# Kernel optimization log

Measured on AMD Instinct MI355X. Metric: run time of the kernel, lower is better.

Reference implementation:

```python
import jax, jax.numpy as jnp
import numpy as np

N, D_IN, D_OUT = 4096, 1024, 1024
DROPOUT_RATE = 0.1


def setup_inputs() -> dict:
    key = jax.random.key(0)
    kx, kq, kk, kv = jax.random.split(key, 4)
    s = 1.0 / np.sqrt(D_IN)
    return {
        "x": jax.random.normal(kx, (N, D_IN), dtype=jnp.float32),
        "wq": jax.random.normal(kq, (D_OUT, D_IN), dtype=jnp.float32) * s,
        "wk": jax.random.normal(kk, (D_OUT, D_IN), dtype=jnp.float32) * s,
        "wv": jax.random.normal(kv, (D_OUT, D_IN), dtype=jnp.float32) * s,
    }


def reference(x, wq, wk, wv):
    # torch Linear: y = x @ W.T  (no bias since qkv_bias=False)
    q = x @ wq.T                      # [N, d_out]
    k = x @ wk.T
    v = x @ wv.T
    scores = q @ k.T                  # [N, N]
    n = scores.shape[0]
    causal = jnp.tril(jnp.ones((n, n), dtype=bool))  # keep lower triangle
    masked = jnp.where(causal, scores, -jnp.inf)
    scale = k.shape[-1] ** 0.5
    weights = jax.nn.softmax(masked / scale, axis=-1)
    # dropout (train mode), fixed key for determinism
    keep = jax.random.bernoulli(jax.random.key(42), 1.0 - DROPOUT_RATE, weights.shape)
    weights = jnp.where(keep, weights / (1.0 - DROPOUT_RATE), 0.0)
    return weights @ v                # [N, d_out]
```

## Files before the change

### kernel.cpp

```cpp
#include <hip/hip_runtime.h>
#include <hip/hip_fp16.h>

typedef __attribute__((ext_vector_type(8))) _Float16 f16x8;
typedef __attribute__((ext_vector_type(4))) float f32x4;

typedef const __attribute__((address_space(1))) void gas_void;
typedef __attribute__((address_space(3))) void las_void;
typedef __attribute__((address_space(3))) const __half las_chalf;

__device__ __forceinline__ f16x8 ldsr(const __half* p) {
    f16x8 r;
    asm volatile("ds_read_b128 %0, %1" : "=v"(r) : "v"((las_chalf*)p));
    return r;
}

__global__ __launch_bounds__(256) void cast_all_k(const float* __restrict__ x,
                                                  const float* __restrict__ wq,
                                                  const float* __restrict__ wk,
                                                  const float* __restrict__ wv,
                                                  __half* __restrict__ xb,
                                                  __half* __restrict__ wqkv) {
    const int b = blockIdx.x;
    const float* src;
    __half* dst;
    size_t i;
    if (b < 2048) {
        src = x; dst = xb;
        i = ((size_t)b * 256 + threadIdx.x) * 8;
    } else {
        const int w = (b - 2048) >> 9;
        src = w == 0 ? wq : (w == 1 ? wk : wv);
        dst = wqkv + (size_t)w * 1048576;
        i = (((size_t)((b - 2048) & 511)) * 256 + threadIdx.x) * 8;
    }
    float4 a = *(const float4*)(src + i);
    float4 c = *(const float4*)(src + i + 4);
    __half2 h[4] = { __floats2half2_rn(a.x, a.y), __floats2half2_rn(a.z, a.w),
                     __floats2half2_rn(c.x, c.y), __floats2half2_rn(c.z, c.w) };
    *(int4*)(dst + i) = *(int4*)h;
}

template <int MODE>
__global__ __launch_bounds__(512, 2)
void gemm256(const __half* __restrict__ pA, const __half* __restrict__ pB,
             void* __restrict__ pC, void* __restrict__ pC2,
             float* __restrict__ P1, float* __restrict__ P2, float* __restrict__ P3,
             const float* __restrict__ Lr) {
    constexpr int LDA = (MODE == 0) ? 1024 : (MODE == 1 ? 2048 : 4096);
    constexpr int LDB = (MODE == 0) ? 1024 : (MODE == 1 ? 2048 : 4096);
    constexpr float SCALE = (MODE == 1) ? 0.03125f : 1.0f;

    int bi, bj, c = 0, k_lo = 0, NT = 16;
    bool isVT = false;
    if constexpr (MODE == 0) {
        const int id = blockIdx.x;
        const int sw = (id & 7) * 24 + (id >> 3);
        if (sw < 128) { bi = sw >> 3; bj = sw & 7; }
        else          { int s2 = sw - 128; bi = s2 >> 4; bj = s2 & 15; isVT = true; }
    } else if constexpr (MODE == 1) {
        const int id = blockIdx.x;
        const int sw = (id & 7) * 17 + (id >> 3);
        int b = (int)((sqrtf(8.0f * sw + 1.0f) - 1.0f) * 0.5f);
        while ((b + 1) * (b + 2) / 2 <= sw) ++b;
        while (b * (b + 1) / 2 > sw) --b;
        bi = b; bj = sw - b * (b + 1) / 2;
    } else {
        const int id = blockIdx.x;
        const int sw = (id & 7) * 20 + (id >> 3);
        bj = sw / 40;
        const int x = sw - 40 * bj;
        if (x < 4)       { bi = x;                    c = 0; }
        else if (x < 12) { bi = 4  + ((x - 4) >> 1);  c = (x - 4) & 1; }
        else if (x < 24) { bi = 8  + (x - 12) / 3;    c = (x - 12) % 3; }
        else             { bi = 12 + ((x - 24) >> 2); c = (x - 24) & 3; }
        const int full = 4 * (bi + 1);
        k_lo = c * 16;
        NT = min(full - k_lo, 16);
    }

    const __half* A = pA;
    const __half* B = pB;
    if constexpr (MODE == 0) {
        if (isVT) { A = pB + 2097152; B = pA; }
    }

    const int brow = bi * 256, bcol = bj * 256;
    const int tid = threadIdx.x;
    const int lane = tid & 63, wid = tid >> 6;
    const int wm = wid >> 2, wn = wid & 3;
    const int lane15 = lane & 15;
    const int kxor = (lane & 7) << 3;
    const int g16 = (lane >> 4) << 3;

    extern __shared__ __half smem[];

    const int srow = (wid << 3) + (lane >> 3);
    const int scol = ((lane & 7) ^ ((lane >> 3) & 7)) << 3;

    auto stage_half = [&](const __half* G, int ldg, int growbase, int kt, int buf, int mat, int half) {
        const __half* src = G + (size_t)(growbase + half * 128 + srow) * ldg + kt * 64 + scol;
        __half* dst = &smem[buf * 32768 + mat * 16384 + (half * 128 + (wid << 3)) * 64];
        __builtin_amdgcn_global_load_lds((gas_void*)src, (las_void*)dst, 16, 0, 0);
        __builtin_amdgcn_global_load_lds((gas_void*)(src + (size_t)64 * ldg),
                                         (las_void*)(dst + 64 * 64), 16, 0, 0);
    };

    f32x4 acc[8][4] = {};
    f16x8 bfrag[2][4];

    stage_half(B, LDB, bcol, k_lo, 0, 1, 0);
    stage_half(B, LDB, bcol, k_lo, 0, 1, 1);
    stage_half(A, LDA, brow, k_lo, 0, 0, 0);
    stage_half(A, LDA, brow, k_lo, 0, 0, 1);
    if (NT > 1) {
        stage_half(B, LDB, bcol, k_lo + 1, 1, 1, 0);
        stage_half(B, LDB, bcol, k_lo + 1, 1, 1, 1);
    }

    for (int Tr = 0; Tr < NT; ++Tr) {
        const int Ta = k_lo + Tr;
        const int buf = Tr & 1;
        const __half* Abase = &smem[buf * 32768 + (wm * 128 + lane15) * 64];
        const __half* Bbase = &smem[buf * 32768 + 16384 + (wn * 64 + lane15) * 64];

        if (Tr < NT - 1) asm volatile("s_waitcnt vmcnt(4)" ::: "memory");
        else             asm volatile("s_waitcnt vmcnt(0)" ::: "memory");
        __builtin_amdgcn_s_barrier();

        {
#pragma unroll
            for (int kk = 0; kk < 2; ++kk)
#pragma unroll
                for (int n = 0; n < 4; ++n)
                    bfrag[kk][n] = ldsr(Bbase + (n * 16) * 64 + ((kk * 32 + g16) ^ kxor));
            f16x8 af[2][2];
#pragma unroll
            for (int mi = 0; mi < 2; ++mi)
#pragma unroll
                for (int kk = 0; kk < 2; ++kk)
                    af[mi][kk] = ldsr(Abase + (mi * 16) * 64 + ((kk * 32 + g16) ^ kxor));
            if (Tr + 1 < NT) stage_half(A, LDA, brow, Ta + 1, buf ^ 1, 0, 0);
            asm volatile("s_waitcnt lgkmcnt(0)" ::: "memory");
            __builtin_amdgcn_sched_barrier(0);
            __builtin_amdgcn_s_setprio(1);
#pragma unroll
            for (int mi = 0; mi < 2; ++mi)
#pragma unroll
                for (int n = 0; n < 4; ++n)
#pragma unroll
                    for (int kk = 0; kk < 2; ++kk)
                        acc[mi][n] = __builtin_amdgcn_mfma_f32_16x16x32_f16(
                            af[mi][kk], bfrag[kk][n], acc[mi][n], 0, 0, 0);
            __builtin_amdgcn_s_setprio(0);
            __builtin_amdgcn_s_barrier();
        }

#pragma unroll
        for (int p = 1; p < 4; ++p) {
            f16x8 af[2][2];
#pragma unroll
            for (int mi = 0; mi < 2; ++mi)
#pragma unroll
                for (int kk = 0; kk < 2; ++kk)
                    af[mi][kk] = ldsr(Abase + ((2 * p + mi) * 16) * 64 + ((kk * 32 + g16) ^ kxor));
            if (p == 1)      { if (Tr + 1 < NT) stage_half(A, LDA, brow, Ta + 1, buf ^ 1, 0, 1); }
            else if (p == 2) { if (Tr + 2 < NT) stage_half(B, LDB, bcol, Ta + 2, buf, 1, 0); }
            else             { if (Tr + 2 < NT) stage_half(B, LDB, bcol, Ta + 2, buf, 1, 1); }
            asm volatile("s_waitcnt lgkmcnt(0)" ::: "memory");
            __builtin_amdgcn_sched_barrier(0);
            __builtin_amdgcn_s_setprio(1);
#pragma unroll
            for (int mi = 0; mi < 2; ++mi)
#pragma unroll
                for (int n = 0; n < 4; ++n)
#pragma unroll
                    for (int kk = 0; kk < 2; ++kk)
                        acc[2 * p + mi][n] = __builtin_amdgcn_mfma_f32_16x16x32_f16(
                            af[mi][kk], bfrag[kk][n], acc[2 * p + mi][n], 0, 0, 0);
            __builtin_amdgcn_s_setprio(0);
            __builtin_amdgcn_s_barrier();
        }
    }

    const int r0 = (lane >> 4) << 2;
    if constexpr (MODE == 2) {
        float* Ct = (float*)pC;
        if (c == 1) Ct = P1; else if (c == 2) Ct = P2; else if (c == 3) Ct = P3;
        const bool doScale = (c == 0) && (bi < 4);
#pragma unroll
        for (int m = 0; m < 8; ++m) {
#pragma unroll
            for (int r = 0; r < 4; ++r) {
                const int row = brow + wm * 128 + m * 16 + r0 + r;
                const float inv = doScale ? 1.0f / (0.9f * Lr[row]) : 1.0f;
#pragma unroll
                for (int n = 0; n < 4; ++n) {
                    const int col = bcol + wn * 64 + n * 16 + lane15;
                    Ct[(size_t)row * 1024 + col] = acc[m][n][r] * inv;
                }
            }
        }
    } else {
        __half* Ct = (__half*)pC;
        int ldc = (MODE == 1) ? 4096 : 2048;
        if constexpr (MODE == 0) {
            if (isVT) { Ct = (__half*)pC2; ldc = 4096; }
        }
#pragma unroll
        for (int m = 0; m < 8; ++m) {
#pragma unroll
            for (int n = 0; n < 4; ++n) {
                const int col = bcol + wn * 64 + n * 16 + lane15;
#pragma unroll
                for (int r = 0; r < 4; ++r) {
                    const int row = brow + wm * 128 + m * 16 + r0 + r;
                    Ct[(size_t)row * ldc + col] = __float2half(acc[m][n][r] * SCALE);
                }
            }
        }
    }
}

__global__ __launch_bounds__(256) void pv_scale_reduce_k(float* __restrict__ out,
                                                         const float* __restrict__ P1,
                                                         const float* __restrict__ P2,
                                                         const float* __restrict__ P3,
                                                         const float* __restrict__ L) {
    const int row = 1024 + blockIdx.x;
    const float inv = 1.0f / (0.9f * L[row]);
    const size_t o = (size_t)row * 1024 + threadIdx.x * 4;
    float4 s = *(float4*)(out + o);
    float4 a = *(const float4*)(P1 + o);
    s.x += a.x; s.y += a.y; s.z += a.z; s.w += a.w;
    if (row >= 2048) {
        float4 b = *(const float4*)(P2 + o);
        s.x += b.x; s.y += b.y; s.z += b.z; s.w += b.w;
    }
    if (row >= 3072) {
        float4 d = *(const float4*)(P3 + o);
        s.x += d.x; s.y += d.y; s.z += d.z; s.w += d.w;
    }
    s.x *= inv; s.y *= inv; s.z *= inv; s.w *= inv;
    *(float4*)(out + o) = s;
}

__device__ __forceinline__ uint32_t rotl32(uint32_t x, int d) { return (x << d) | (x >> (32 - d)); }

__device__ __forceinline__ bool keep_bit(uint32_t flat) {
    uint32_t x0 = 0u;
    uint32_t x1 = flat;
    const uint32_t ks0 = 0u, ks1 = 42u, ks2 = 0u ^ 42u ^ 0x1BD11BDAu;
    x0 += ks0; x1 += ks1;
#define TFR(r) { x0 += x1; x1 = rotl32(x1, r); x1 ^= x0; }
    TFR(13) TFR(15) TFR(26) TFR(6)   x0 += ks1; x1 += ks2 + 1u;
    TFR(17) TFR(29) TFR(16) TFR(24)  x0 += ks2; x1 += ks0 + 2u;
    TFR(13) TFR(15) TFR(26) TFR(6)   x0 += ks0; x1 += ks1 + 3u;
    TFR(17) TFR(29) TFR(16) TFR(24)  x0 += ks1; x1 += ks2 + 4u;
    TFR(13) TFR(15) TFR(26) TFR(6)   x0 += ks2; x1 += ks0 + 5u;
#undef TFR
    uint32_t bits = x0 ^ x1;
    float u = __uint_as_float((bits >> 9) | 0x3f800000u) - 1.0f;
    return u < 0.9f;
}

__global__ __launch_bounds__(256) void softdrop_k(__half* __restrict__ SP,
                                                  float* __restrict__ L, int N) {
    const int i = blockIdx.x;
    const int tid = threadIdx.x;
    const int len = i + 1;
    __half* row = SP + (size_t)i * N;

    float l = 0.f;
    const int len8 = len & ~7;
    for (int j = tid * 8; j < len8; j += 2048) {
        int4 pk = *(const int4*)(row + j);
        const __half* hp = (const __half*)&pk;
        __half o8[8];
        const uint32_t base = (uint32_t)i * 4096u + (uint32_t)j;
#pragma unroll
        for (int q = 0; q < 8; ++q) {
            float e = __expf(__half2float(hp[q]));
            l += e;
            o8[q] = keep_bit(base + q) ? __float2half(e) : __float2half(0.0f);
        }
        *(int4*)(row + j) = *(int4*)o8;
    }
    for (int j = len8 + tid; j < len; j += 256) {
        float e = __expf(__half2float(row[j]));
        l += e;
        row[j] = keep_bit((uint32_t)i * 4096u + (uint32_t)j) ? __float2half(e) : __float2half(0.0f);
    }

    for (int off = 1; off < 64; off <<= 1) l += __shfl_xor(l, off);
    __shared__ float ls[4];
    if ((tid & 63) == 0) ls[tid >> 6] = l;
    __syncthreads();
    if (tid == 0) L[i] = ls[0] + ls[1] + ls[2] + ls[3];

    const int zlim = ((i >> 8) << 8) + 256;
    const int za = (len + 7) & ~7;
    for (int j = len + tid; j < min(za, zlim); j += 256) row[j] = __float2half(0.0f);
    const int4 z = {0, 0, 0, 0};
    for (int j = za + tid * 8; j < zlim; j += 2048) *(int4*)(row + j) = z;
}

extern "C" void kernel_launch(void* const* d_in, const int* in_sizes, int n_in,
                              void* d_out, int out_size, void* d_ws, size_t ws_size,
                              hipStream_t stream) {
    const float* x  = (const float*)d_in[0];
    const float* wq = (const float*)d_in[1];
    const float* wk = (const float*)d_in[2];
    const float* wv = (const float*)d_in[3];
    float* out = (float*)d_out;
    char* ws = (char*)d_ws;

    const int N = 4096, D = 1024;

    __half* xb   = (__half*)(ws + 0);
    __half* wqkv = (__half*)(ws + 8388608);
    __half* QK   = (__half*)(ws + 14680064);
    __half* VT   = (__half*)(ws + 31457280);
    __half* SP   = (__half*)(ws + 48234496);
    float*  Lr   = (float*)(ws + 81788928);

    float* P1 = (float*)(ws + 14680064) - (size_t)1024 * 1024;
    float* P3 = (float*)(ws + 27262976) - (size_t)3072 * 1024;
    float* P2 = (float*)(ws + 39845888) - (size_t)2048 * 1024;

    __half* Q = QK;
    __half* K = QK + 1024;

    auto* g0 = gemm256<0>;
    auto* g1 = gemm256<1>;
    auto* g2 = gemm256<2>;
    (void)hipFuncSetAttribute((const void*)g0, hipFuncAttributeMaxDynamicSharedMemorySize, 131072);
    (void)hipFuncSetAttribute((const void*)g1, hipFuncAttributeMaxDynamicSharedMemorySize, 131072);
    (void)hipFuncSetAttribute((const void*)g2, hipFuncAttributeMaxDynamicSharedMemorySize, 131072);

    cast_all_k<<<3584, 256, 0, stream>>>(x, wq, wk, wv, xb, wqkv);

    g0<<<192, 512, 131072, stream>>>(xb, wqkv, QK, VT, nullptr, nullptr, nullptr, nullptr);

    g1<<<136, 512, 131072, stream>>>(Q, K, SP, nullptr, nullptr, nullptr, nullptr, nullptr);

    softdrop_k<<<N, 256, 0, stream>>>(SP, Lr, N);

    g2<<<160, 512, 131072, stream>>>(SP, VT, out, nullptr, P1, P2, P3, Lr);

    pv_scale_reduce_k<<<3072, 256, 0, stream>>>(out, P1, P2, P3, Lr);
}
```

Before: 145.5 us.

## Fuse all stages into one cooperative persistent kernel with grid syncs

Replaces the six separate launches (cast, QKV GEMM, QK^T GEMM, softmax+dropout, PV GEMM, reduce) with a single cooperative kernel of 256 blocks that runs each stage and separates them with grid.sync(). The GEMM main loop moves into a shared device function so the fallback kernels and the mega kernel use the same code. The aim is to remove launch gaps and inter-kernel idle time. In exchange, each stage is limited to 256 blocks, and some stages leave blocks idle (for example only 136 of 256 work in QK^T). The softmax stage now processes many rows per block with 512 threads, and the grid syncs add their own overhead.

```diff
diff --git a/kernel.cpp b/kernel.cpp
--- a/kernel.cpp
+++ b/kernel.cpp
@@ -1,5 +1,8 @@
 #include <hip/hip_runtime.h>
 #include <hip/hip_fp16.h>
+#include <hip/hip_cooperative_groups.h>
+
+namespace cg = cooperative_groups;
 
 typedef __attribute__((ext_vector_type(8))) _Float16 f16x8;
 typedef __attribute__((ext_vector_type(4))) float f32x4;
@@ -12,6 +15,326 @@
     f16x8 r;
     asm volatile("ds_read_b128 %0, %1" : "=v"(r) : "v"((las_chalf*)p));
     return r;
+}
+
+__device__ __forceinline__ uint32_t rotl32(uint32_t x, int d) { return (x << d) | (x >> (32 - d)); }
+
+__device__ __forceinline__ bool keep_bit(uint32_t flat) {
+    uint32_t x0 = 0u;
+    uint32_t x1 = flat;
+    const uint32_t ks0 = 0u, ks1 = 42u, ks2 = 0u ^ 42u ^ 0x1BD11BDAu;
+    x0 += ks0; x1 += ks1;
+#define TFR(r) { x0 += x1; x1 = rotl32(x1, r); x1 ^= x0; }
+    TFR(13) TFR(15) TFR(26) TFR(6)   x0 += ks1; x1 += ks2 + 1u;
+    TFR(17) TFR(29) TFR(16) TFR(24)  x0 += ks2; x1 += ks0 + 2u;
+    TFR(13) TFR(15) TFR(26) TFR(6)   x0 += ks0; x1 += ks1 + 3u;
+    TFR(17) TFR(29) TFR(16) TFR(24)  x0 += ks1; x1 += ks2 + 4u;
+    TFR(13) TFR(15) TFR(26) TFR(6)   x0 += ks2; x1 += ks0 + 5u;
+#undef TFR
+    uint32_t bits = x0 ^ x1;
+    float u = __uint_as_float((bits >> 9) | 0x3f800000u) - 1.0f;
+    return u < 0.9f;
+}
+
+template <int LD>
+__device__ __forceinline__ void gemm_core(const __half* __restrict__ A, const __half* __restrict__ B,
+                                          int brow, int bcol, int k_lo, int NT,
+                                          __half* smem, f32x4 (&acc)[8][4]) {
+    const int tid = threadIdx.x;
+    const int lane = tid & 63, wid = tid >> 6;
+    const int wm = wid >> 2, wn = wid & 3;
+    const int lane15 = lane & 15;
+    const int kxor = (lane & 7) << 3;
+    const int g16 = (lane >> 4) << 3;
+
+    const int srow = (wid << 3) + (lane >> 3);
+    const int scol = ((lane & 7) ^ ((lane >> 3) & 7)) << 3;
+
+    auto stage_half = [&](const __half* G, int growbase, int kt, int buf, int mat, int half) {
+        const __half* src = G + (size_t)(growbase + half * 128 + srow) * LD + kt * 64 + scol;
+        __half* dst = &smem[buf * 32768 + mat * 16384 + (half * 128 + (wid << 3)) * 64];
+        __builtin_amdgcn_global_load_lds((gas_void*)src, (las_void*)dst, 16, 0, 0);
+        __builtin_amdgcn_global_load_lds((gas_void*)(src + (size_t)64 * LD),
+                                         (las_void*)(dst + 64 * 64), 16, 0, 0);
+    };
+
+    f16x8 bfrag[2][4];
+
+    stage_half(B, bcol, k_lo, 0, 1, 0);
+    stage_half(B, bcol, k_lo, 0, 1, 1);
+    stage_half(A, brow, k_lo, 0, 0, 0);
+    stage_half(A, brow, k_lo, 0, 0, 1);
+    if (NT > 1) {
+        stage_half(B, bcol, k_lo + 1, 1, 1, 0);
+        stage_half(B, bcol, k_lo + 1, 1, 1, 1);
+    }
+
+    for (int Tr = 0; Tr < NT; ++Tr) {
+        const int Ta = k_lo + Tr;
+        const int buf = Tr & 1;
+        const __half* Abase = &smem[buf * 32768 + (wm * 128 + lane15) * 64];
+        const __half* Bbase = &smem[buf * 32768 + 16384 + (wn * 64 + lane15) * 64];
+
+        if (Tr < NT - 1) asm volatile("s_waitcnt vmcnt(4)" ::: "memory");
+        else             asm volatile("s_waitcnt vmcnt(0)" ::: "memory");
+        __builtin_amdgcn_s_barrier();
+
+        {
+#pragma unroll
+            for (int kk = 0; kk < 2; ++kk)
+#pragma unroll
+                for (int n = 0; n < 4; ++n)
+                    bfrag[kk][n] = ldsr(Bbase + (n * 16) * 64 + ((kk * 32 + g16) ^ kxor));
+            f16x8 af[2][2];
+#pragma unroll
+            for (int mi = 0; mi < 2; ++mi)
+#pragma unroll
+                for (int kk = 0; kk < 2; ++kk)
+                    af[mi][kk] = ldsr(Abase + (mi * 16) * 64 + ((kk * 32 + g16) ^ kxor));
+            if (Tr + 1 < NT) stage_half(A, brow, Ta + 1, buf ^ 1, 0, 0);
+            asm volatile("s_waitcnt lgkmcnt(0)" ::: "memory");
+            __builtin_amdgcn_sched_barrier(0);
+            __builtin_amdgcn_s_setprio(1);
+#pragma unroll
+            for (int mi = 0; mi < 2; ++mi)
+#pragma unroll
+                for (int n = 0; n < 4; ++n)
+#pragma unroll
+                    for (int kk = 0; kk < 2; ++kk)
+                        acc[mi][n] = __builtin_amdgcn_mfma_f32_16x16x32_f16(
+                            af[mi][kk], bfrag[kk][n], acc[mi][n], 0, 0, 0);
+            __builtin_amdgcn_s_setprio(0);
+            __builtin_amdgcn_s_barrier();
+        }
+
+#pragma unroll
+        for (int p = 1; p < 4; ++p) {
+            f16x8 af[2][2];
+#pragma unroll
+            for (int mi = 0; mi < 2; ++mi)
+#pragma unroll
+                for (int kk = 0; kk < 2; ++kk)
+                    af[mi][kk] = ldsr(Abase + ((2 * p + mi) * 16) * 64 + ((kk * 32 + g16) ^ kxor));
+            if (p == 1)      { if (Tr + 1 < NT) stage_half(A, brow, Ta + 1, buf ^ 1, 0, 1); }
+            else if (p == 2) { if (Tr + 2 < NT) stage_half(B, bcol, Ta + 2, buf, 1, 0); }
+            else             { if (Tr + 2 < NT) stage_half(B, bcol, Ta + 2, buf, 1, 1); }
+            asm volatile("s_waitcnt lgkmcnt(0)" ::: "memory");
+            __builtin_amdgcn_sched_barrier(0);
+            __builtin_amdgcn_s_setprio(1);
+#pragma unroll
+            for (int mi = 0; mi < 2; ++mi)
+#pragma unroll
+                for (int n = 0; n < 4; ++n)
+#pragma unroll
+                    for (int kk = 0; kk < 2; ++kk)
+                        acc[2 * p + mi][n] = __builtin_amdgcn_mfma_f32_16x16x32_f16(
+                            af[mi][kk], bfrag[kk][n], acc[2 * p + mi][n], 0, 0, 0);
+            __builtin_amdgcn_s_setprio(0);
+            __builtin_amdgcn_s_barrier();
+        }
+    }
+}
+
+__global__ __launch_bounds__(512, 2)
+void mega_k(const float* __restrict__ x, const float* __restrict__ wq,
+            const float* __restrict__ wk, const float* __restrict__ wv,
+            __half* __restrict__ xb, __half* __restrict__ wqkv,
+            __half* __restrict__ QK, __half* __restrict__ VT,
+            __half* __restrict__ SP, float* __restrict__ Lr,
+            float* __restrict__ out,
+            float* __restrict__ P1, float* __restrict__ P2, float* __restrict__ P3) {
+    cg::grid_group grid = cg::this_grid();
+    extern __shared__ __half smem[];
+
+    const int id = blockIdx.x;
+    const int tid = threadIdx.x;
+    const int role = (id & 7) * 32 + (id >> 3);
+    const int gtid = id * 512 + tid;
+
+    {
+        for (int t = gtid; t < 524288; t += 131072) {
+            const size_t i = (size_t)t * 8;
+            float4 a = *(const float4*)(x + i);
+            float4 c = *(const float4*)(x + i + 4);
+            __half2 h[4] = { __floats2half2_rn(a.x, a.y), __floats2half2_rn(a.z, a.w),
+                             __floats2half2_rn(c.x, c.y), __floats2half2_rn(c.z, c.w) };
+            *(int4*)(xb + i) = *(int4*)h;
+        }
+        for (int t = gtid; t < 393216; t += 131072) {
+            const size_t i = (size_t)t * 8;
+            const int w = (int)(i >> 20);
+            const float* src = w == 0 ? wq : (w == 1 ? wk : wv);
+            const size_t off = i & 1048575u;
+            float4 a = *(const float4*)(src + off);
+            float4 c = *(const float4*)(src + off + 4);
+            __half2 h[4] = { __floats2half2_rn(a.x, a.y), __floats2half2_rn(a.z, a.w),
+                             __floats2half2_rn(c.x, c.y), __floats2half2_rn(c.z, c.w) };
+            *(int4*)(wqkv + i) = *(int4*)h;
+        }
+    }
+    grid.sync();
+
+    const int lane = tid & 63, wid = tid >> 6;
+    const int wm = wid >> 2, wn = wid & 3;
+    const int lane15 = lane & 15;
+    const int r0 = (lane >> 4) << 2;
+
+    if (role < 192) {
+        f32x4 acc[8][4] = {};
+        if (role < 128) {
+            const int bi = role >> 3, bj = role & 7;
+            gemm_core<1024>(xb, wqkv, bi * 256, bj * 256, 0, 16, smem, acc);
+#pragma unroll
+            for (int m = 0; m < 8; ++m)
+#pragma unroll
+                for (int n = 0; n < 4; ++n) {
+                    const int col = bj * 256 + wn * 64 + n * 16 + lane15;
+#pragma unroll
+                    for (int r = 0; r < 4; ++r) {
+                        const int row = bi * 256 + wm * 128 + m * 16 + r0 + r;
+                        QK[(size_t)row * 2048 + col] = __float2half(acc[m][n][r]);
+                    }
+                }
+        } else {
+            const int s2 = role - 128;
+            const int bi = s2 >> 4, bj = s2 & 15;
+            gemm_core<1024>(wqkv + 2097152, xb, bi * 256, bj * 256, 0, 16, smem, acc);
+#pragma unroll
+            for (int m = 0; m < 8; ++m)
+#pragma unroll
+                for (int n = 0; n < 4; ++n) {
+                    const int col = bj * 256 + wn * 64 + n * 16 + lane15;
+#pragma unroll
+                    for (int r = 0; r < 4; ++r) {
+                        const int row = bi * 256 + wm * 128 + m * 16 + r0 + r;
+                        VT[(size_t)row * 4096 + col] = __float2half(acc[m][n][r]);
+                    }
+                }
+        }
+    }
+    grid.sync();
+
+    if (role < 136) {
+        int b = (int)((sqrtf(8.0f * role + 1.0f) - 1.0f) * 0.5f);
+        while ((b + 1) * (b + 2) / 2 <= role) ++b;
+        while (b * (b + 1) / 2 > role) --b;
+        const int bi = b, bj = role - b * (b + 1) / 2;
+        f32x4 acc[8][4] = {};
+        gemm_core<2048>(QK, QK + 1024, bi * 256, bj * 256, 0, 16, smem, acc);
+#pragma unroll
+        for (int m = 0; m < 8; ++m)
+#pragma unroll
+            for (int n = 0; n < 4; ++n) {
+                const int col = bj * 256 + wn * 64 + n * 16 + lane15;
+#pragma unroll
+                for (int r = 0; r < 4; ++r) {
+                    const int row = bi * 256 + wm * 128 + m * 16 + r0 + r;
+                    SP[(size_t)row * 4096 + col] = __float2half(acc[m][n][r] * 0.03125f);
+                }
+            }
+    }
+    grid.sync();
+
+    {
+        float* ls = (float*)smem;
+        for (int i = id; i < 4096; i += 256) {
+            const int len = i + 1;
+            __half* row = SP + (size_t)i * 4096;
+
+            float l = 0.f;
+            const int len8 = len & ~7;
+            for (int j = tid * 8; j < len8; j += 4096) {
+                int4 pk = *(const int4*)(row + j);
+                const __half* hp = (const __half*)&pk;
+                __half o8[8];
+                const uint32_t base = (uint32_t)i * 4096u + (uint32_t)j;
+#pragma unroll
+                for (int q = 0; q < 8; ++q) {
+                    float e = __expf(__half2float(hp[q]));
+                    l += e;
+                    o8[q] = keep_bit(base + q) ? __float2half(e) : __float2half(0.0f);
+                }
+                *(int4*)(row + j) = *(int4*)o8;
+            }
+            for (int j = len8 + tid; j < len; j += 512) {
+                float e = __expf(__half2float(row[j]));
+                l += e;
+                row[j] = keep_bit((uint32_t)i * 4096u + (uint32_t)j) ? __float2half(e)
+                                                                     : __float2half(0.0f);
+            }
+
+            for (int off = 1; off < 64; off <<= 1) l += __shfl_xor(l, off);
+            if (lane == 0) ls[wid] = l;
+            __syncthreads();
+            if (tid == 0) {
+                float s = 0.f;
+#pragma unroll
+                for (int w = 0; w < 8; ++w) s += ls[w];
+                Lr[i] = s;
+            }
+
+            const int zlim = ((i >> 8) << 8) + 256;
+            const int za = (len + 7) & ~7;
+            for (int j = len + tid; j < min(za, zlim); j += 512) row[j] = __float2half(0.0f);
+            const int4 z = {0, 0, 0, 0};
+            for (int j = za + tid * 8; j < zlim; j += 4096) *(int4*)(row + j) = z;
+            __syncthreads();
+        }
+    }
+    grid.sync();
+
+    if (role < 160) {
+        const int bj = role / 40;
+        const int xr = role - 40 * bj;
+        int bi, c;
+        if (xr < 4)       { bi = xr;                     c = 0; }
+        else if (xr < 12) { bi = 4  + ((xr - 4) >> 1);   c = (xr - 4) & 1; }
+        else if (xr < 24) { bi = 8  + (xr - 12) / 3;     c = (xr - 12) % 3; }
+        else              { bi = 12 + ((xr - 24) >> 2);  c = (xr - 24) & 3; }
+        const int full = 4 * (bi + 1);
+        const int k_lo = c * 16;
+        const int NT = min(full - k_lo, 16);
+
+        f32x4 acc[8][4] = {};
+        gemm_core<4096>(SP, VT, bi * 256, bj * 256, k_lo, NT, smem, acc);
+
+        float* Ct = out;
+        if (c == 1) Ct = P1; else if (c == 2) Ct = P2; else if (c == 3) Ct = P3;
+        const bool doScale = (c == 0) && (bi < 4);
+#pragma unroll
+        for (int m = 0; m < 8; ++m)
+#pragma unroll
+            for (int r = 0; r < 4; ++r) {
+                const int row = bi * 256 + wm * 128 + m * 16 + r0 + r;
+                const float inv = doScale ? 1.0f / (0.9f * Lr[row]) : 1.0f;
+#pragma unroll
+                for (int n = 0; n < 4; ++n) {
+                    const int col = bj * 256 + wn * 64 + n * 16 + lane15;
+                    Ct[(size_t)row * 1024 + col] = acc[m][n][r] * inv;
+                }
+            }
+    }
+    grid.sync();
+
+    for (int it = 0; it < 6; ++it) {
+        const int row = 1024 + id * 12 + it * 2 + (tid >> 8);
+        const int cv = tid & 255;
+        const float inv = 1.0f / (0.9f * Lr[row]);
+        const size_t o = (size_t)row * 1024 + cv * 4;
+        float4 s = *(float4*)(out + o);
+        float4 a = *(const float4*)(P1 + o);
+        s.x += a.x; s.y += a.y; s.z += a.z; s.w += a.w;
+        if (row >= 2048) {
+            float4 b2 = *(const float4*)(P2 + o);
+            s.x += b2.x; s.y += b2.y; s.z += b2.z; s.w += b2.w;
+        }
+        if (row >= 3072) {
+            float4 d = *(const float4*)(P3 + o);
+            s.x += d.x; s.y += d.y; s.z += d.z; s.w += d.w;
+        }
+        s.x *= inv; s.y *= inv; s.z *= inv; s.w *= inv;
+        *(float4*)(out + o) = s;
+    }
 }
 
 __global__ __launch_bounds__(256) void cast_all_k(const float* __restrict__ x,
@@ -46,10 +369,6 @@
              void* __restrict__ pC, void* __restrict__ pC2,
              float* __restrict__ P1, float* __restrict__ P2, float* __restrict__ P3,
              const float* __restrict__ Lr) {
-    constexpr int LDA = (MODE == 0) ? 1024 : (MODE == 1 ? 2048 : 4096);
-    constexpr int LDB = (MODE == 0) ? 1024 : (MODE == 1 ? 2048 : 4096);
-    constexpr float SCALE = (MODE == 1) ? 0.03125f : 1.0f;
-
     int bi, bj, c = 0, k_lo = 0, NT = 16;
     bool isVT = false;
     if constexpr (MODE == 0) {
@@ -68,11 +387,11 @@
         const int id = blockIdx.x;
         const int sw = (id & 7) * 20 + (id >> 3);
         bj = sw / 40;
-        const int x = sw - 40 * bj;
-        if (x < 4)       { bi = x;                    c = 0; }
-        else if (x < 12) { bi = 4  + ((x - 4) >> 1);  c = (x - 4) & 1; }
-        else if (x < 24) { bi = 8  + (x - 12) / 3;    c = (x - 12) % 3; }
-        else             { bi = 12 + ((x - 24) >> 2); c = (x - 24) & 3; }
+        const int xr = sw - 40 * bj;
+        if (xr < 4)       { bi = xr;                     c = 0; }
+        else if (xr < 12) { bi = 4  + ((xr - 4) >> 1);   c = (xr - 4) & 1; }
+        else if (xr < 24) { bi = 8  + (xr - 12) / 3;     c = (xr - 12) % 3; }
+        else              { bi = 12 + ((xr - 24) >> 2);  c = (xr - 24) & 3; }
         const int full = 4 * (bi + 1);
         k_lo = c * 16;
         NT = min(full - k_lo, 16);
@@ -84,140 +403,51 @@
         if (isVT) { A = pB + 2097152; B = pA; }
     }
 
-    const int brow = bi * 256, bcol = bj * 256;
+    extern __shared__ __half smem[];
+    f32x4 acc[8][4] = {};
+    constexpr int LD = (MODE == 0) ? 1024 : (MODE == 1 ? 2048 : 4096);
+    gemm_core<LD>(A, B, bi * 256, bj * 256, k_lo, NT, smem, acc);
+
     const int tid = threadIdx.x;
     const int lane = tid & 63, wid = tid >> 6;
     const int wm = wid >> 2, wn = wid & 3;
     const int lane15 = lane & 15;
-    const int kxor = (lane & 7) << 3;
-    const int g16 = (lane >> 4) << 3;
-
-    extern __shared__ __half smem[];
-
-    const int srow = (wid << 3) + (lane >> 3);
-    const int scol = ((lane & 7) ^ ((lane >> 3) & 7)) << 3;
-
-    auto stage_half = [&](const __half* G, int ldg, int growbase, int kt, int buf, int mat, int half) {
-        const __half* src = G + (size_t)(growbase + half * 128 + srow) * ldg + kt * 64 + scol;
-        __half* dst = &smem[buf * 32768 + mat * 16384 + (half * 128 + (wid << 3)) * 64];
-        __builtin_amdgcn_global_load_lds((gas_void*)src, (las_void*)dst, 16, 0, 0);
-        __builtin_amdgcn_global_load_lds((gas_void*)(src + (size_t)64 * ldg),
-                                         (las_void*)(dst + 64 * 64), 16, 0, 0);
-    };
-
-    f32x4 acc[8][4] = {};
-    f16x8 bfrag[2][4];
-
-    stage_half(B, LDB, bcol, k_lo, 0, 1, 0);
-    stage_half(B, LDB, bcol, k_lo, 0, 1, 1);
-    stage_half(A, LDA, brow, k_lo, 0, 0, 0);
-    stage_half(A, LDA, brow, k_lo, 0, 0, 1);
-    if (NT > 1) {
-        stage_half(B, LDB, bcol, k_lo + 1, 1, 1, 0);
-        stage_half(B, LDB, bcol, k_lo + 1, 1, 1, 1);
-    }
-
-    for (int Tr = 0; Tr < NT; ++Tr) {
-        const int Ta = k_lo + Tr;
-        const int buf = Tr & 1;
-        const __half* Abase = &smem[buf * 32768 + (wm * 128 + lane15) * 64];
-        const __half* Bbase = &smem[buf * 32768 + 16384 + (wn * 64 + lane15) * 64];
-
-        if (Tr < NT - 1) asm volatile("s_waitcnt vmcnt(4)" ::: "memory");
-        else             asm volatile("s_waitcnt vmcnt(0)" ::: "memory");
-        __builtin_amdgcn_s_barrier();
-
-        {
-#pragma unroll
-            for (int kk = 0; kk < 2; ++kk)
-#pragma unroll
-                for (int n = 0; n < 4; ++n)
-                    bfrag[kk][n] = ldsr(Bbase + (n * 16) * 64 + ((kk * 32 + g16) ^ kxor));
-            f16x8 af[2][2];
-#pragma unroll
-            for (int mi = 0; mi < 2; ++mi)
-#pragma unroll
-                for (int kk = 0; kk < 2; ++kk)
-                    af[mi][kk] = ldsr(Abase + (mi * 16) * 64 + ((kk * 32 + g16) ^ kxor));
-            if (Tr + 1 < NT) stage_half(A, LDA, brow, Ta + 1, buf ^ 1, 0, 0);
-            asm volatile("s_waitcnt lgkmcnt(0)" ::: "memory");
-            __builtin_amdgcn_sched_barrier(0);
-            __builtin_amdgcn_s_setprio(1);
-#pragma unroll
-            for (int mi = 0; mi < 2; ++mi)
-#pragma unroll
-                for (int n = 0; n < 4; ++n)
-#pragma unroll
-                    for (int kk = 0; kk < 2; ++kk)
-                        acc[mi][n] = __builtin_amdgcn_mfma_f32_16x16x32_f16(
-                            af[mi][kk], bfrag[kk][n], acc[mi][n], 0, 0, 0);
-            __builtin_amdgcn_s_setprio(0);
-            __builtin_amdgcn_s_barrier();
-        }
-
-#pragma unroll
-        for (int p = 1; p < 4; ++p) {
-            f16x8 af[2][2];
-#pragma unroll
-            for (int mi = 0; mi < 2; ++mi)
-#pragma unroll
-                for (int kk = 0; kk < 2; ++kk)
-                    af[mi][kk] = ldsr(Abase + ((2 * p + mi) * 16) * 64 + ((kk * 32 + g16) ^ kxor));
-            if (p == 1)      { if (Tr + 1 < NT) stage_half(A, LDA, brow, Ta + 1, buf ^ 1, 0, 1); }
-            else if (p == 2) { if (Tr + 2 < NT) stage_half(B, LDB, bcol, Ta + 2, buf, 1, 0); }
-            else             { if (Tr + 2 < NT) stage_half(B, LDB, bcol, Ta + 2, buf, 1, 1); }
-            asm volatile("s_waitcnt lgkmcnt(0)" ::: "memory");
-            __builtin_amdgcn_sched_barrier(0);
-            __builtin_amdgcn_s_setprio(1);
-#pragma unroll
-            for (int mi = 0; mi < 2; ++mi)
-#pragma unroll
-                for (int n = 0; n < 4; ++n)
-#pragma unroll
-                    for (int kk = 0; kk < 2; ++kk)
-                        acc[2 * p + mi][n] = __builtin_amdgcn_mfma_f32_16x16x32_f16(
-                            af[mi][kk], bfrag[kk][n], acc[2 * p + mi][n], 0, 0, 0);
-            __builtin_amdgcn_s_setprio(0);
-            __builtin_amdgcn_s_barrier();
-        }
-    }
-
     const int r0 = (lane >> 4) << 2;
+
     if constexpr (MODE == 2) {
         float* Ct = (float*)pC;
         if (c == 1) Ct = P1; else if (c == 2) Ct = P2; else if (c == 3) Ct = P3;
         const bool doScale = (c == 0) && (bi < 4);
 #pragma unroll
-        for (int m = 0; m < 8; ++m) {
+        for (int m = 0; m < 8; ++m)
 #pragma unroll
             for (int r = 0; r < 4; ++r) {
-                const int row = brow + wm * 128 + m * 16 + r0 + r;
+                const int row = bi * 256 + wm * 128 + m * 16 + r0 + r;
                 const float inv = doScale ? 1.0f / (0.9f * Lr[row]) : 1.0f;
 #pragma unroll
                 for (int n = 0; n < 4; ++n) {
-                    const int col = bcol + wn * 64 + n * 16 + lane15;
+                    const int col = bj * 256 + wn * 64 + n * 16 + lane15;
                     Ct[(size_t)row * 1024 + col] = acc[m][n][r] * inv;
                 }
             }
-        }
     } else {
         __half* Ct = (__half*)pC;
         int ldc = (MODE == 1) ? 4096 : 2048;
+        float scl = (MODE == 1) ? 0.03125f : 1.0f;
         if constexpr (MODE == 0) {
             if (isVT) { Ct = (__half*)pC2; ldc = 4096; }
         }
 #pragma unroll
-        for (int m = 0; m < 8; ++m) {
+        for (int m = 0; m < 8; ++m)
 #pragma unroll
             for (int n = 0; n < 4; ++n) {
-                const int col = bcol + wn * 64 + n * 16 + lane15;
+                const int col = bj * 256 + wn * 64 + n * 16 + lane15;
 #pragma unroll
                 for (int r = 0; r < 4; ++r) {
-                    const int row = brow + wm * 128 + m * 16 + r0 + r;
-                    Ct[(size_t)row * ldc + col] = __float2half(acc[m][n][r] * SCALE);
-                }
-            }
-        }
+                    const int row = bi * 256 + wm * 128 + m * 16 + r0 + r;
+                    Ct[(size_t)row * ldc + col] = __float2half(acc[m][n][r] * scl);
+                }
+            }
     }
 }
 
@@ -244,25 +474,6 @@
     *(float4*)(out + o) = s;
 }
 
-__device__ __forceinline__ uint32_t rotl32(uint32_t x, int d) { return (x << d) | (x >> (32 - d)); }
-
-__device__ __forceinline__ bool keep_bit(uint32_t flat) {
-    uint32_t x0 = 0u;
-    uint32_t x1 = flat;
-    const uint32_t ks0 = 0u, ks1 = 42u, ks2 = 0u ^ 42u ^ 0x1BD11BDAu;
-    x0 += ks0; x1 += ks1;
-#define TFR(r) { x0 += x1; x1 = rotl32(x1, r); x1 ^= x0; }
-    TFR(13) TFR(15) TFR(26) TFR(6)   x0 += ks1; x1 += ks2 + 1u;
-    TFR(17) TFR(29) TFR(16) TFR(24)  x0 += ks2; x1 += ks0 + 2u;
-    TFR(13) TFR(15) TFR(26) TFR(6)   x0 += ks0; x1 += ks1 + 3u;
-    TFR(17) TFR(29) TFR(16) TFR(24)  x0 += ks1; x1 += ks2 + 4u;
-    TFR(13) TFR(15) TFR(26) TFR(6)   x0 += ks2; x1 += ks0 + 5u;
-#undef TFR
-    uint32_t bits = x0 ^ x1;
-    float u = __uint_as_float((bits >> 9) | 0x3f800000u) - 1.0f;
-    return u < 0.9f;
-}
-
 __global__ __launch_bounds__(256) void softdrop_k(__half* __restrict__ SP,
                                                   float* __restrict__ L, int N) {
     const int i = blockIdx.x;
@@ -314,7 +525,7 @@
     float* out = (float*)d_out;
     char* ws = (char*)d_ws;
 
-    const int N = 4096, D = 1024;
+    const int N = 4096;
 
     __half* xb   = (__half*)(ws + 0);
     __half* wqkv = (__half*)(ws + 8388608);
@@ -327,6 +538,16 @@
     float* P3 = (float*)(ws + 27262976) - (size_t)3072 * 1024;
     float* P2 = (float*)(ws + 39845888) - (size_t)2048 * 1024;
 
+    (void)hipFuncSetAttribute((const void*)mega_k, hipFuncAttributeMaxDynamicSharedMemorySize, 131072);
+
+    void* args[] = { (void*)&x, (void*)&wq, (void*)&wk, (void*)&wv,
+                     (void*)&xb, (void*)&wqkv, (void*)&QK, (void*)&VT,
+                     (void*)&SP, (void*)&Lr, (void*)&out,
+                     (void*)&P1, (void*)&P2, (void*)&P3 };
+    hipError_t err = hipLaunchCooperativeKernel((const void*)mega_k, dim3(256), dim3(512),
+                                                args, 131072, stream);
+    if (err == hipSuccess) return;
+
     __half* Q = QK;
     __half* K = QK + 1024;
 
@@ -338,14 +559,9 @@
     (void)hipFuncSetAttribute((const void*)g2, hipFuncAttributeMaxDynamicSharedMemorySize, 131072);
 
     cast_all_k<<<3584, 256, 0, stream>>>(x, wq, wk, wv, xb, wqkv);
-
     g0<<<192, 512, 131072, stream>>>(xb, wqkv, QK, VT, nullptr, nullptr, nullptr, nullptr);
-
     g1<<<136, 512, 131072, stream>>>(Q, K, SP, nullptr, nullptr, nullptr, nullptr, nullptr);
-
     softdrop_k<<<N, 256, 0, stream>>>(SP, Lr, N);
-
     g2<<<160, 512, 131072, stream>>>(SP, VT, out, nullptr, P1, P2, P3, Lr);
-
     pv_scale_reduce_k<<<3072, 256, 0, stream>>>(out, P1, P2, P3, Lr);
 }
```

Measured after the change: 306.7 us. +110.8%, slower.

## Rebalance causal PV split-K into 13-tile chunks with fp16 partial planes

Applied to the files above, without the earlier changes.

The split-K decomposition of the causal P·V GEMM changes from 16-tile chunks (160 blocks) to 13-tile chunks (196 blocks), so work spreads more evenly across CUs. Partial sums for the non-first chunks are now stored as fp16 in dedicated workspace planes instead of fp32. The merge kernel reads a variable number of planes per row. The intent is better load balance and less partial-sum traffic, at the cost of fp16 rounding on the partials and one more partial plane.

```diff
diff --git a/kernel.cpp b/kernel.cpp
--- a/kernel.cpp
+++ b/kernel.cpp
@@ -44,11 +44,10 @@
 __global__ __launch_bounds__(512, 2)
 void gemm256(const __half* __restrict__ pA, const __half* __restrict__ pB,
              void* __restrict__ pC, void* __restrict__ pC2,
-             float* __restrict__ P1, float* __restrict__ P2, float* __restrict__ P3,
+             __half* __restrict__ PH1, __half* __restrict__ PH2,
+             __half* __restrict__ PH3, __half* __restrict__ PH4,
              const float* __restrict__ Lr) {
-    constexpr int LDA = (MODE == 0) ? 1024 : (MODE == 1 ? 2048 : 4096);
-    constexpr int LDB = (MODE == 0) ? 1024 : (MODE == 1 ? 2048 : 4096);
-    constexpr float SCALE = (MODE == 1) ? 0.03125f : 1.0f;
+    constexpr int LD = (MODE == 0) ? 1024 : (MODE == 1 ? 2048 : 4096);
 
     int bi, bj, c = 0, k_lo = 0, NT = 16;
     bool isVT = false;
@@ -66,16 +65,19 @@
         bi = b; bj = sw - b * (b + 1) / 2;
     } else {
         const int id = blockIdx.x;
-        const int sw = (id & 7) * 20 + (id >> 3);
-        bj = sw / 40;
-        const int x = sw - 40 * bj;
-        if (x < 4)       { bi = x;                    c = 0; }
-        else if (x < 12) { bi = 4  + ((x - 4) >> 1);  c = (x - 4) & 1; }
-        else if (x < 24) { bi = 8  + (x - 12) / 3;    c = (x - 12) % 3; }
-        else             { bi = 12 + ((x - 24) >> 2); c = (x - 24) & 3; }
+        const int xcd = id & 7;
+        const int sw = (xcd < 4 ? xcd * 25 : 100 + (xcd - 4) * 24) + (id >> 3);
+        bj = sw / 49;
+        int x = sw - 49 * bj;
+        int nch = 1;
+        for (bi = 0; bi < 16; ++bi) {
+            nch = (4 * (bi + 1) + 12) / 13;
+            if (x < nch) { c = x; break; }
+            x -= nch;
+        }
         const int full = 4 * (bi + 1);
-        k_lo = c * 16;
-        NT = min(full - k_lo, 16);
+        k_lo = c * 13;
+        NT = min(full - k_lo, 13);
     }
 
     const __half* A = pA;
@@ -97,24 +99,24 @@
     const int srow = (wid << 3) + (lane >> 3);
     const int scol = ((lane & 7) ^ ((lane >> 3) & 7)) << 3;
 
-    auto stage_half = [&](const __half* G, int ldg, int growbase, int kt, int buf, int mat, int half) {
-        const __half* src = G + (size_t)(growbase + half * 128 + srow) * ldg + kt * 64 + scol;
+    auto stage_half = [&](const __half* G, int growbase, int kt, int buf, int mat, int half) {
+        const __half* src = G + (size_t)(growbase + half * 128 + srow) * LD + kt * 64 + scol;
         __half* dst = &smem[buf * 32768 + mat * 16384 + (half * 128 + (wid << 3)) * 64];
         __builtin_amdgcn_global_load_lds((gas_void*)src, (las_void*)dst, 16, 0, 0);
-        __builtin_amdgcn_global_load_lds((gas_void*)(src + (size_t)64 * ldg),
+        __builtin_amdgcn_global_load_lds((gas_void*)(src + (size_t)64 * LD),
                                          (las_void*)(dst + 64 * 64), 16, 0, 0);
     };
 
     f32x4 acc[8][4] = {};
     f16x8 bfrag[2][4];
 
-    stage_half(B, LDB, bcol, k_lo, 0, 1, 0);
-    stage_half(B, LDB, bcol, k_lo, 0, 1, 1);
-    stage_half(A, LDA, brow, k_lo, 0, 0, 0);
-    stage_half(A, LDA, brow, k_lo, 0, 0, 1);
+    stage_half(B, bcol, k_lo, 0, 1, 0);
+    stage_half(B, bcol, k_lo, 0, 1, 1);
+    stage_half(A, brow, k_lo, 0, 0, 0);
+    stage_half(A, brow, k_lo, 0, 0, 1);
     if (NT > 1) {
-        stage_half(B, LDB, bcol, k_lo + 1, 1, 1, 0);
-        stage_half(B, LDB, bcol, k_lo + 1, 1, 1, 1);
+        stage_half(B, bcol, k_lo + 1, 1, 1, 0);
+        stage_half(B, bcol, k_lo + 1, 1, 1, 1);
     }
 
     for (int Tr = 0; Tr < NT; ++Tr) {
@@ -139,7 +141,7 @@
 #pragma unroll
                 for (int kk = 0; kk < 2; ++kk)
                     af[mi][kk] = ldsr(Abase + (mi * 16) * 64 + ((kk * 32 + g16) ^ kxor));
-            if (Tr + 1 < NT) stage_half(A, LDA, brow, Ta + 1, buf ^ 1, 0, 0);
+            if (Tr + 1 < NT) stage_half(A, brow, Ta + 1, buf ^ 1, 0, 0);
             asm volatile("s_waitcnt lgkmcnt(0)" ::: "memory");
             __builtin_amdgcn_sched_barrier(0);
             __builtin_amdgcn_s_setprio(1);
@@ -163,9 +165,9 @@
 #pragma unroll
                 for (int kk = 0; kk < 2; ++kk)
                     af[mi][kk] = ldsr(Abase + ((2 * p + mi) * 16) * 64 + ((kk * 32 + g16) ^ kxor));
-            if (p == 1)      { if (Tr + 1 < NT) stage_half(A, LDA, brow, Ta + 1, buf ^ 1, 0, 1); }
-            else if (p == 2) { if (Tr + 2 < NT) stage_half(B, LDB, bcol, Ta + 2, buf, 1, 0); }
-            else             { if (Tr + 2 < NT) stage_half(B, LDB, bcol, Ta + 2, buf, 1, 1); }
+            if (p == 1)      { if (Tr + 1 < NT) stage_half(A, brow, Ta + 1, buf ^ 1, 0, 1); }
+            else if (p == 2) { if (Tr + 2 < NT) stage_half(B, bcol, Ta + 2, buf, 1, 0); }
+            else             { if (Tr + 2 < NT) stage_half(B, bcol, Ta + 2, buf, 1, 1); }
             asm volatile("s_waitcnt lgkmcnt(0)" ::: "memory");
             __builtin_amdgcn_sched_barrier(0);
             __builtin_amdgcn_s_setprio(1);
@@ -184,61 +186,75 @@
 
     const int r0 = (lane >> 4) << 2;
     if constexpr (MODE == 2) {
-        float* Ct = (float*)pC;
-        if (c == 1) Ct = P1; else if (c == 2) Ct = P2; else if (c == 3) Ct = P3;
-        const bool doScale = (c == 0) && (bi < 4);
-#pragma unroll
-        for (int m = 0; m < 8; ++m) {
-#pragma unroll
-            for (int r = 0; r < 4; ++r) {
-                const int row = brow + wm * 128 + m * 16 + r0 + r;
-                const float inv = doScale ? 1.0f / (0.9f * Lr[row]) : 1.0f;
+        if (c == 0) {
+            float* Ct = (float*)pC;
+            const bool doScale = (4 * (bi + 1) <= 13);
+#pragma unroll
+            for (int m = 0; m < 8; ++m)
+#pragma unroll
+                for (int r = 0; r < 4; ++r) {
+                    const int row = brow + wm * 128 + m * 16 + r0 + r;
+                    const float inv = doScale ? 1.0f / (0.9f * Lr[row]) : 1.0f;
+#pragma unroll
+                    for (int n = 0; n < 4; ++n) {
+                        const int col = bcol + wn * 64 + n * 16 + lane15;
+                        Ct[(size_t)row * 1024 + col] = acc[m][n][r] * inv;
+                    }
+                }
+        } else {
+            __half* Ph = (c == 1) ? PH1 : (c == 2 ? PH2 : (c == 3 ? PH3 : PH4));
+#pragma unroll
+            for (int m = 0; m < 8; ++m)
 #pragma unroll
                 for (int n = 0; n < 4; ++n) {
                     const int col = bcol + wn * 64 + n * 16 + lane15;
-                    Ct[(size_t)row * 1024 + col] = acc[m][n][r] * inv;
+#pragma unroll
+                    for (int r = 0; r < 4; ++r) {
+                        const int row = brow + wm * 128 + m * 16 + r0 + r;
+                        Ph[(size_t)row * 1024 + col] = __float2half(acc[m][n][r]);
+                    }
                 }
-            }
         }
     } else {
         __half* Ct = (__half*)pC;
         int ldc = (MODE == 1) ? 4096 : 2048;
+        const float scl = (MODE == 1) ? 0.03125f : 1.0f;
         if constexpr (MODE == 0) {
             if (isVT) { Ct = (__half*)pC2; ldc = 4096; }
         }
 #pragma unroll
-        for (int m = 0; m < 8; ++m) {
+        for (int m = 0; m < 8; ++m)
 #pragma unroll
             for (int n = 0; n < 4; ++n) {
                 const int col = bcol + wn * 64 + n * 16 + lane15;
 #pragma unroll
                 for (int r = 0; r < 4; ++r) {
                     const int row = brow + wm * 128 + m * 16 + r0 + r;
-                    Ct[(size_t)row * ldc + col] = __float2half(acc[m][n][r] * SCALE);
+                    Ct[(size_t)row * ldc + col] = __float2half(acc[m][n][r] * scl);
                 }
             }
-        }
-    }
-}
-
-__global__ __launch_bounds__(256) void pv_scale_reduce_k(float* __restrict__ out,
-                                                         const float* __restrict__ P1,
-                                                         const float* __restrict__ P2,
-                                                         const float* __restrict__ P3,
-                                                         const float* __restrict__ L) {
-    const int row = 1024 + blockIdx.x;
+    }
+}
+
+__global__ __launch_bounds__(256) void pv_merge_k(float* __restrict__ out,
+                                                  const __half* __restrict__ PH1,
+                                                  const __half* __restrict__ PH2,
+                                                  const __half* __restrict__ PH3,
+                                                  const __half* __restrict__ PH4,
+                                                  const float* __restrict__ L) {
+    const int row = 768 + blockIdx.x;
+    const int bi = row >> 8;
+    const int nch = (4 * (bi + 1) + 12) / 13;
     const float inv = 1.0f / (0.9f * L[row]);
     const size_t o = (size_t)row * 1024 + threadIdx.x * 4;
     float4 s = *(float4*)(out + o);
-    float4 a = *(const float4*)(P1 + o);
-    s.x += a.x; s.y += a.y; s.z += a.z; s.w += a.w;
-    if (row >= 2048) {
-        float4 b = *(const float4*)(P2 + o);
-        s.x += b.x; s.y += b.y; s.z += b.z; s.w += b.w;
-    }
-    if (row >= 3072) {
-        float4 d = *(const float4*)(P3 + o);
-        s.x += d.x; s.y += d.y; s.z += d.z; s.w += d.w;
+    const __half* planes[4] = { PH1, PH2, PH3, PH4 };
+#pragma unroll 4
+    for (int cc = 1; cc < nch; ++cc) {
+        const __half2* p2 = (const __half2*)(planes[cc - 1] + o);
+        float2 a = __half22float2(p2[0]);
+        float2 b = __half22float2(p2[1]);
+        s.x += a.x; s.y += a.y; s.z += b.x; s.w += b.y;
     }
     s.x *= inv; s.y *= inv; s.z *= inv; s.w *= inv;
     *(float4*)(out + o) = s;
@@ -314,7 +330,7 @@
     float* out = (float*)d_out;
     char* ws = (char*)d_ws;
 
-    const int N = 4096, D = 1024;
+    const int N = 4096;
 
     __half* xb   = (__half*)(ws + 0);
     __half* wqkv = (__half*)(ws + 8388608);
@@ -322,10 +338,10 @@
     __half* VT   = (__half*)(ws + 31457280);
     __half* SP   = (__half*)(ws + 48234496);
     float*  Lr   = (float*)(ws + 81788928);
-
-    float* P1 = (float*)(ws + 14680064) - (size_t)1024 * 1024;
-    float* P3 = (float*)(ws + 27262976) - (size_t)3072 * 1024;
-    float* P2 = (float*)(ws + 39845888) - (size_t)2048 * 1024;
+    __half* PH1  = (__half*)(ws + 83886080);
+    __half* PH2  = (__half*)(ws + 92274688);
+    __half* PH3  = (__half*)(ws + 100663296);
+    __half* PH4  = (__half*)(ws + 109051904);
 
     __half* Q = QK;
     __half* K = QK + 1024;
@@ -339,13 +355,13 @@
 
     cast_all_k<<<3584, 256, 0, stream>>>(x, wq, wk, wv, xb, wqkv);
 
-    g0<<<192, 512, 131072, stream>>>(xb, wqkv, QK, VT, nullptr, nullptr, nullptr, nullptr);
-
-    g1<<<136, 512, 131072, stream>>>(Q, K, SP, nullptr, nullptr, nullptr, nullptr, nullptr);
+    g0<<<192, 512, 131072, stream>>>(xb, wqkv, QK, VT, nullptr, nullptr, nullptr, nullptr, nullptr);
+
+    g1<<<136, 512, 131072, stream>>>(Q, K, SP, nullptr, nullptr, nullptr, nullptr, nullptr, nullptr);
 
     softdrop_k<<<N, 256, 0, stream>>>(SP, Lr, N);
 
-    g2<<<160, 512, 131072, stream>>>(SP, VT, out, nullptr, P1, P2, P3, Lr);
-
-    pv_scale_reduce_k<<<3072, 256, 0, stream>>>(out, P1, P2, P3, Lr);
-}
+    g2<<<196, 512, 131072, stream>>>(SP, VT, out, nullptr, PH1, PH2, PH3, PH4, Lr);
+
+    pv_merge_k<<<3328, 256, 0, stream>>>(out, PH1, PH2, PH3, PH4, Lr);
+}
```

Result: faster. 139.3 us (-4.2%).
